# Kernel tuning notes

Measured on AMD Instinct MI355X. Metric: run time of the kernel, lower is better.

Reference implementation:

```python
import jax, jax.numpy as jnp
import numpy as np

N_IN, N_UP, N_OUT = 65536, 262144, 131072
C_IN, C_OUT = 128, 64
K1, K2, K3 = 27, 27, 16      # kernel offsets: 3x3x3x1, 3x3x3x1, 2x2x2x2
M1, M2, M3 = 65536, 131072, 131072  # gather/scatter pairs per offset
EPS = 1e-6
ALPHA = 0.0


def setup_inputs() -> dict:
    key = jax.random.key(0)
    ks = jax.random.split(key, 13)
    return {
        "input_feats": jax.random.normal(ks[0], (N_IN, C_IN), jnp.float32),
        "encoder_feats": jax.random.normal(ks[1], (N_UP, C_OUT), jnp.float32),
        "W1t": jax.random.normal(ks[2], (K1, C_IN, C_OUT), jnp.float32) * 0.05,
        "W2": jax.random.normal(ks[3], (K2, C_OUT, C_OUT), jnp.float32) * 0.05,
        "W3": jax.random.normal(ks[4], (K3, C_OUT, C_OUT), jnp.float32) * 0.05,
        "Wp": jax.random.normal(ks[5], (C_OUT, 1), jnp.float32) * 0.05,
        "bp": jnp.zeros((1,), jnp.float32),
        "kin1": jax.random.randint(ks[6], (K1, M1), 0, N_IN, jnp.int32),
        "kout1": jax.random.randint(ks[7], (K1, M1), 0, N_UP, jnp.int32),
        "kin2": jax.random.randint(ks[8], (K2, M2), 0, N_UP, jnp.int32),
        "kout2": jax.random.randint(ks[9], (K2, M2), 0, N_UP, jnp.int32),
        "kin3": jax.random.randint(ks[10], (K3, M3), 0, N_UP, jnp.int32),
        "kout3": jax.random.randint(ks[11], (K3, M3), 0, N_OUT, jnp.int32),
        "n_out": N_OUT,
    }


def _sparse_conv(x, W, kin, kout, n_out):
    """Kernel-map gather-GEMM-scatter sparse conv.
    x: [N_in, Cin]; W: [K, Cin, Cout]; kin/kout: [K, M] index pairs."""
    y = jnp.einsum('kmc,kcd->kmd', x[kin], W)  # gather + per-offset GEMM
    out = jnp.zeros((n_out, W.shape[-1]), x.dtype)
    return out.at[kout].add(y)                 # scatter-accumulate


def _inorm(x):
    # MinkowskiInstanceNorm, single batch instance: per-channel over points
    mu = x.mean(0, keepdims=True)
    var = x.var(0, keepdims=True)
    return (x - mu) * jax.lax.rsqrt(var + EPS)


def reference(input_feats, encoder_feats, W1t, W2, W3, Wp, bp,
              kin1, kout1, kin2, kout2, kin3, kout3, n_out):
    n_up = encoder_feats.shape[0]
    # dec_block_1: gen conv-transpose 3x3x3x1 s2 -> IN -> ELU -> conv 3x3x3x1 -> IN -> ELU
    x = _sparse_conv(input_feats, W1t, kin1, kout1, n_up)
    x = jax.nn.elu(_inorm(x))
    x = _sparse_conv(x, W2, kin2, kout2, n_up)
    x = jax.nn.elu(_inorm(x))
    # skip connection
    x = x + encoder_feats
    # dec_block_2: conv k=2 stride [1,1,1,2] -> IN -> ELU
    x = _sparse_conv(x, W3, kin3, kout3, n_out)
    x = jax.nn.elu(_inorm(x))
    # 1x1 pruning conv (bias=True) + threshold keep mask
    pruning = x @ Wp + bp                      # [N_OUT, 1]
    keep = pruning[:, 0] > ALPHA
    # MinkowskiPruning gathers kept rows (dynamic shape); static-shape
    # equivalent: zero out pruned rows and return the mask.
    return x * keep[:, None].astype(x.dtype), keep
```

## Files before the change

kernel.cpp:

```cpp
#include <hip/hip_runtime.h>
#include <math.h>

#define N_IN   65536
#define N_UP   262144
#define N_OUT  131072
#define C_IN   128
#define C_OUT  64
#define K1     27
#define K2     27
#define K3     16
#define M1     65536
#define M2     131072
#define M3     131072
#define EPSV   1e-6f
#define WPK    256
#define WPK_SHIFT 8

template <int CIN, int R>
__global__ __launch_bounds__(256) void conv_scatter_reg(
    const float* __restrict__ X, const float* __restrict__ W,
    const int* __restrict__ kin, const int* __restrict__ kout,
    float* __restrict__ outp)
{
    const int lane = threadIdx.x & 63;
    const int wave = blockIdx.x * 4 + (threadIdx.x >> 6);
    const int k    = wave >> WPK_SHIFT;
    const int widx = wave & (WPK - 1);

    float wreg[CIN];
    {
        const float* wk = W + (size_t)k * (CIN * 64) + lane;
#pragma unroll
        for (int i = 0; i < CIN; ++i) wreg[i] = wk[i * 64];
    }

    const long long rbase = (long long)k * (WPK * R) + (long long)widx * R;
    const int* kin_p  = kin + rbase;
    const int* kout_p = kout + rbase;

#pragma unroll 2
    for (int rr = 0; rr < R; ++rr) {
        const int src = __builtin_amdgcn_readfirstlane(kin_p[rr]);
        const int dst = __builtin_amdgcn_readfirstlane(kout_p[rr]);
        const float* xr = X + (size_t)src * CIN;
        float a0 = 0.f, a1 = 0.f, a2 = 0.f, a3 = 0.f;
#pragma unroll
        for (int i = 0; i < CIN; i += 4) {
            a0 = fmaf(xr[i + 0], wreg[i + 0], a0);
            a1 = fmaf(xr[i + 1], wreg[i + 1], a1);
            a2 = fmaf(xr[i + 2], wreg[i + 2], a2);
            a3 = fmaf(xr[i + 3], wreg[i + 3], a3);
        }
        atomicAdd(outp + (size_t)dst * 64 + lane, (a0 + a1) + (a2 + a3));
    }
}

__global__ __launch_bounds__(256) void stats_kernel(
    const float* __restrict__ x, int nrows, float* __restrict__ stats)
{
    __shared__ float sh[2][4][64];
    const int c  = threadIdx.x & 63;
    const int rw = threadIdx.x >> 6;
    float s = 0.f, s2 = 0.f;
    for (int r = blockIdx.x * 4 + rw; r < nrows; r += gridDim.x * 4) {
        float v = x[(size_t)r * 64 + c];
        s += v;
        s2 = fmaf(v, v, s2);
    }
    sh[0][rw][c] = s;
    sh[1][rw][c] = s2;
    __syncthreads();
    if (rw == 0) {
        s  = (sh[0][0][c] + sh[0][1][c]) + (sh[0][2][c] + sh[0][3][c]);
        s2 = (sh[1][0][c] + sh[1][1][c]) + (sh[1][2][c] + sh[1][3][c]);
        atomicAdd(stats + c, s);
        atomicAdd(stats + 64 + c, s2);
    }
}

__global__ void finalize_stats(float* stats, float inv_n)
{
    const int c = threadIdx.x;
    float mu  = stats[c] * inv_n;
    float var = stats[64 + c] * inv_n - mu * mu;
    stats[128 + c] = mu;
    stats[192 + c] = rsqrtf(var + EPSV);
}

__global__ __launch_bounds__(256) void norm_elu(
    float* __restrict__ x, const float* __restrict__ stats,
    const float* __restrict__ enc)
{
    const int i = blockIdx.x * 256 + threadIdx.x;
    const int c = i & 63;
    float v = (x[i] - stats[128 + c]) * stats[192 + c];
    v = (v > 0.f) ? v : expm1f(v);
    if (enc) v += enc[i];
    x[i] = v;
}

__global__ __launch_bounds__(256) void final_kernel(
    const float* __restrict__ x, const float* __restrict__ stats,
    const float* __restrict__ Wp, const float* __restrict__ bp,
    float* __restrict__ outp)
{
    const int lane = threadIdx.x & 63;
    const int wid  = threadIdx.x >> 6;
    const int row  = blockIdx.x * 4 + wid;

    float v = (x[(size_t)row * 64 + lane] - stats[128 + lane]) * stats[192 + lane];
    v = (v > 0.f) ? v : expm1f(v);

    float p = v * Wp[lane];
#pragma unroll
    for (int m = 1; m < 64; m <<= 1)
        p += __shfl_xor(p, m, 64);
    p += bp[0];

    const bool keep = p > 0.0f;
    outp[(size_t)row * 64 + lane] = keep ? v : 0.f;
    if (lane == 0)
        outp[(size_t)N_OUT * 64 + row] = keep ? 1.f : 0.f;
}

extern "C" void kernel_launch(void* const* d_in, const int* in_sizes, int n_in,
                              void* d_out, int out_size, void* d_ws, size_t ws_size,
                              hipStream_t stream)
{
    const float* in_feats = (const float*)d_in[0];
    const float* enc      = (const float*)d_in[1];
    const float* W1       = (const float*)d_in[2];
    const float* W2       = (const float*)d_in[3];
    const float* W3       = (const float*)d_in[4];
    const float* Wp       = (const float*)d_in[5];
    const float* bp       = (const float*)d_in[6];
    const int* kin1  = (const int*)d_in[7];
    const int* kout1 = (const int*)d_in[8];
    const int* kin2  = (const int*)d_in[9];
    const int* kout2 = (const int*)d_in[10];
    const int* kin3  = (const int*)d_in[11];
    const int* kout3 = (const int*)d_in[12];
    float* outp = (float*)d_out;

    char* ws = (char*)d_ws;
    float* up_a   = (float*)ws;
    float* up_b   = (float*)(ws + 67108864);
    float* out3   = up_a;
    float* statsA = (float*)(ws + 134217728);
    float* statsB = statsA + 256;
    float* statsC = statsA + 512;

    hipMemsetAsync(up_a, 0, (size_t)N_UP * 64 * 4, stream);
    hipMemsetAsync(up_b, 0, (size_t)N_UP * 64 * 4, stream);
    hipMemsetAsync(statsA, 0, 3 * 256 * 4, stream);

    conv_scatter_reg<128, M1 / WPK><<<(K1 * WPK) / 4, 256, 0, stream>>>(
        in_feats, W1, kin1, kout1, up_a);
    stats_kernel<<<512, 256, 0, stream>>>(up_a, N_UP, statsA);
    finalize_stats<<<1, 64, 0, stream>>>(statsA, 1.f / N_UP);
    norm_elu<<<(N_UP * 64) / 256, 256, 0, stream>>>(up_a, statsA, nullptr);

    conv_scatter_reg<64, M2 / WPK><<<(K2 * WPK) / 4, 256, 0, stream>>>(
        up_a, W2, kin2, kout2, up_b);
    stats_kernel<<<512, 256, 0, stream>>>(up_b, N_UP, statsB);
    finalize_stats<<<1, 64, 0, stream>>>(statsB, 1.f / N_UP);
    norm_elu<<<(N_UP * 64) / 256, 256, 0, stream>>>(up_b, statsB, enc);

    hipMemsetAsync(out3, 0, (size_t)N_OUT * 64 * 4, stream);
    conv_scatter_reg<64, M3 / WPK><<<(K3 * WPK) / 4, 256, 0, stream>>>(
        up_b, W3, kin3, kout3, out3);
    stats_kernel<<<512, 256, 0, stream>>>(out3, N_OUT, statsC);
    finalize_stats<<<1, 64, 0, stream>>>(statsC, 1.f / N_OUT);

    final_kernel<<<N_OUT / 4, 256, 0, stream>>>(out3, statsC, Wp, bp, outp);
}
```

Before: 2.770 ms.

## Restructure sparse conv to row-per-lane GEMM with LDS-transposed coalesced atomics

Each lane now owns one gathered row and computes all 64 output channels in a register accumulator, streaming the input row as float4 loads with one-chunk prefetch. Weights are read as wave-uniform (scalar-broadcast) values instead of being held per lane in registers. Results are transposed through LDS so that atomic scatter-adds write 16 contiguous channels per row. This replaces the per-row, wave-serial dot-product loop, which was latency-bound, with much higher arithmetic density. In exchange it uses many more VGPRs (64 accumulators), which may lower occupancy, and lanes now issue uncoalesced per-row gathers.

```diff
diff --git a/kernel.cpp b/kernel.cpp
--- a/kernel.cpp
+++ b/kernel.cpp
@@ -16,42 +16,87 @@
 #define WPK    256
 #define WPK_SHIFT 8
 
-template <int CIN, int R>
-__global__ __launch_bounds__(256) void conv_scatter_reg(
+template <int CIN, int MSHIFT>
+__global__ __launch_bounds__(256) void conv_gemm(
     const float* __restrict__ X, const float* __restrict__ W,
     const int* __restrict__ kin, const int* __restrict__ kout,
     float* __restrict__ outp)
 {
+    __shared__ float lds_t[4][64][20];
+    __shared__ int   lds_dst[4][64];
+
     const int lane = threadIdx.x & 63;
-    const int wave = blockIdx.x * 4 + (threadIdx.x >> 6);
-    const int k    = wave >> WPK_SHIFT;
+    const int wv   = threadIdx.x >> 6;
+    const int wave = blockIdx.x * 4 + wv;
+    const int k    = __builtin_amdgcn_readfirstlane(wave >> WPK_SHIFT);
     const int widx = wave & (WPK - 1);
-
-    float wreg[CIN];
-    {
-        const float* wk = W + (size_t)k * (CIN * 64) + lane;
-#pragma unroll
-        for (int i = 0; i < CIN; ++i) wreg[i] = wk[i * 64];
-    }
-
-    const long long rbase = (long long)k * (WPK * R) + (long long)widx * R;
-    const int* kin_p  = kin + rbase;
-    const int* kout_p = kout + rbase;
-
-#pragma unroll 2
-    for (int rr = 0; rr < R; ++rr) {
-        const int src = __builtin_amdgcn_readfirstlane(kin_p[rr]);
-        const int dst = __builtin_amdgcn_readfirstlane(kout_p[rr]);
-        const float* xr = X + (size_t)src * CIN;
-        float a0 = 0.f, a1 = 0.f, a2 = 0.f, a3 = 0.f;
-#pragma unroll
-        for (int i = 0; i < CIN; i += 4) {
-            a0 = fmaf(xr[i + 0], wreg[i + 0], a0);
-            a1 = fmaf(xr[i + 1], wreg[i + 1], a1);
-            a2 = fmaf(xr[i + 2], wreg[i + 2], a2);
-            a3 = fmaf(xr[i + 3], wreg[i + 3], a3);
+    constexpr int R  = (1 << MSHIFT) / WPK;
+    constexpr int NB = R / 64;
+    constexpr int KC = CIN / 16;
+
+    const float* Wk = W + (size_t)k * (CIN * 64);
+    const int base = (k << MSHIFT) + widx * R;
+
+    for (int b = 0; b < NB; ++b) {
+        const int j   = base + b * 64 + lane;
+        const int src = kin[j];
+        const int dst = kout[j];
+        lds_dst[wv][lane] = dst;
+
+        const float4* xr = (const float4*)(X + (size_t)src * CIN);
+
+        float acc[64];
+#pragma unroll
+        for (int c = 0; c < 64; ++c) acc[c] = 0.f;
+
+        float4 xa0 = xr[0], xa1 = xr[1], xa2 = xr[2], xa3 = xr[3];
+
+        for (int kc = 0; kc < KC; ++kc) {
+            float4 xb0, xb1, xb2, xb3;
+            if (kc + 1 < KC) {
+                xb0 = xr[(kc + 1) * 4 + 0];
+                xb1 = xr[(kc + 1) * 4 + 1];
+                xb2 = xr[(kc + 1) * 4 + 2];
+                xb3 = xr[(kc + 1) * 4 + 3];
+            }
+            float xs[16];
+            xs[0]=xa0.x; xs[1]=xa0.y; xs[2]=xa0.z; xs[3]=xa0.w;
+            xs[4]=xa1.x; xs[5]=xa1.y; xs[6]=xa1.z; xs[7]=xa1.w;
+            xs[8]=xa2.x; xs[9]=xa2.y; xs[10]=xa2.z; xs[11]=xa2.w;
+            xs[12]=xa3.x; xs[13]=xa3.y; xs[14]=xa3.z; xs[15]=xa3.w;
+
+            const float* wrow = Wk + kc * 16 * 64;
+#pragma unroll
+            for (int i = 0; i < 16; ++i) {
+                const float xi = xs[i];
+                const float* wr = wrow + i * 64;
+#pragma unroll
+                for (int c = 0; c < 64; ++c)
+                    acc[c] = fmaf(xi, wr[c], acc[c]);
+            }
+            xa0 = xb0; xa1 = xb1; xa2 = xb2; xa3 = xb3;
         }
-        atomicAdd(outp + (size_t)dst * 64 + lane, (a0 + a1) + (a2 + a3));
+
+#pragma unroll
+        for (int cc = 0; cc < 4; ++cc) {
+#pragma unroll
+            for (int q = 0; q < 4; ++q) {
+                float4 v;
+                v.x = acc[cc * 16 + q * 4 + 0];
+                v.y = acc[cc * 16 + q * 4 + 1];
+                v.z = acc[cc * 16 + q * 4 + 2];
+                v.w = acc[cc * 16 + q * 4 + 3];
+                *(float4*)&lds_t[wv][lane][q * 4] = v;
+            }
+            const int c16 = lane & 15;
+#pragma unroll
+            for (int t = 0; t < 16; ++t) {
+                const int rr = (lane >> 4) + 4 * t;
+                const float v = lds_t[wv][rr][c16];
+                const int   d = lds_dst[wv][rr];
+                atomicAdd(outp + (size_t)d * 64 + cc * 16 + c16, v);
+            }
+        }
     }
 }
 
@@ -154,20 +199,20 @@
     hipMemsetAsync(up_b, 0, (size_t)N_UP * 64 * 4, stream);
     hipMemsetAsync(statsA, 0, 3 * 256 * 4, stream);
 
-    conv_scatter_reg<128, M1 / WPK><<<(K1 * WPK) / 4, 256, 0, stream>>>(
+    conv_gemm<128, 16><<<(K1 * WPK) / 4, 256, 0, stream>>>(
         in_feats, W1, kin1, kout1, up_a);
     stats_kernel<<<512, 256, 0, stream>>>(up_a, N_UP, statsA);
     finalize_stats<<<1, 64, 0, stream>>>(statsA, 1.f / N_UP);
     norm_elu<<<(N_UP * 64) / 256, 256, 0, stream>>>(up_a, statsA, nullptr);
 
-    conv_scatter_reg<64, M2 / WPK><<<(K2 * WPK) / 4, 256, 0, stream>>>(
+    conv_gemm<64, 17><<<(K2 * WPK) / 4, 256, 0, stream>>>(
         up_a, W2, kin2, kout2, up_b);
     stats_kernel<<<512, 256, 0, stream>>>(up_b, N_UP, statsB);
     finalize_stats<<<1, 64, 0, stream>>>(statsB, 1.f / N_UP);
     norm_elu<<<(N_UP * 64) / 256, 256, 0, stream>>>(up_b, statsB, enc);
 
     hipMemsetAsync(out3, 0, (size_t)N_OUT * 64 * 4, stream);
-    conv_scatter_reg<64, M3 / WPK><<<(K3 * WPK) / 4, 256, 0, stream>>>(
+    conv_gemm<64, 17><<<(K3 * WPK) / 4, 256, 0, stream>>>(
         up_b, W3, kin3, kout3, out3);
     stats_kernel<<<512, 256, 0, stream>>>(out3, N_OUT, statsC);
     finalize_stats<<<1, 64, 0, stream>>>(statsC, 1.f / N_OUT);
```

Result: faster. 2.505 ms (-9.6%).
